# Kernel tuning notes

Measured on AMD Instinct MI355X. Metric: run time of the kernel, lower is better.

Reference implementation:

```python
import jax, jax.numpy as jnp
import numpy as np

N, D, E = 16384, 256, 8
H = D // 2  # gate hidden


def setup_inputs() -> dict:
    key = jax.random.key(0)
    ks = jax.random.split(key, 10)
    s = lambda fan_in: 1.0 / np.sqrt(fan_in)
    return {
        "x":   jax.random.normal(ks[0], (N, D), dtype=jnp.float32),
        # gate: Linear(D, D//2) -> ReLU -> Linear(D//2, E) -> Softmax
        "Wg1": jax.random.uniform(ks[1], (D, H), jnp.float32, -s(D), s(D)),
        "bg1": jax.random.uniform(ks[2], (H,), jnp.float32, -s(D), s(D)),
        "Wg2": jax.random.uniform(ks[3], (H, E), jnp.float32, -s(H), s(H)),
        "bg2": jax.random.uniform(ks[4], (E,), jnp.float32, -s(H), s(H)),
        # experts: per-expert Linear(D,D) -> ReLU -> (Dropout eval=identity) -> Linear(D,D)
        "W1": jax.random.uniform(ks[5], (E, D, D), jnp.float32, -s(D), s(D)),
        "b1": jax.random.uniform(ks[6], (E, D), jnp.float32, -s(D), s(D)),
        "W2": jax.random.uniform(ks[7], (E, D, D), jnp.float32, -s(D), s(D)),
        "b2": jax.random.uniform(ks[8], (E, D), jnp.float32, -s(D), s(D)),
    }


def reference(x, Wg1, bg1, Wg2, bg2, W1, b1, W2, b2):
    # gate: [N, E] softmax over experts
    g = jax.nn.softmax(jax.nn.relu(x @ Wg1 + bg1) @ Wg2 + bg2, axis=-1)
    # all experts applied densely via batched GEMMs (fuses the Python loop)
    h = jax.nn.relu(jnp.einsum("nd,edh->neh", x, W1) + b1)  # [N, E, D]
    y = jnp.einsum("neh,ehd->ned", h, W2) + b2              # [N, E, D]
    # weighted combine: sum_e g[n,e] * y[n,e,:]
    return jnp.einsum("ned,ne->nd", y, g)
```

## Files before the change

### kernel.cpp

```cpp
#include <hip/hip_runtime.h>


typedef unsigned short USH;
typedef float f32x4 __attribute__((ext_vector_type(4)));
typedef __bf16 bf16x8 __attribute__((ext_vector_type(8)));

__device__ __forceinline__ USH f2bf(float f) {
  unsigned int u = __float_as_uint(f);
  u += 0x7fffu + ((u >> 16) & 1u);
  return (USH)(u >> 16);
}


__global__ __launch_bounds__(256) void k_prep(
    const float* __restrict__ Wg1,
    const float* __restrict__ W1,
    const float* __restrict__ W2,
    USH* __restrict__ w1f, USH* __restrict__ w2f, USH* __restrict__ wg1f) {
  __shared__ float T[64][65];
  int b = blockIdx.x, tid = threadIdx.x;

  if (b < 128) {
    int e = b >> 4, tl = b & 15;
    int c0 = (tl >> 2) * 64, h0 = (tl & 3) * 64;
    const float* src = W1 + (size_t)e * 65536;
#pragma unroll
    for (int p = 0; p < 4; ++p) {
      int r = p * 16 + (tid >> 4), d4 = (tid & 15) * 4;
      float4 v = *(const float4*)(src + (size_t)(c0 + r) * 256 + h0 + d4);
      T[r][d4] = v.x; T[r][d4 + 1] = v.y; T[r][d4 + 2] = v.z; T[r][d4 + 3] = v.w;
    }
    __syncthreads();
#pragma unroll
    for (int p = 0; p < 4; ++p) {
      int hr = p * 16 + (tid >> 4), c4 = (tid & 15) * 4;
      USH w[4];
#pragma unroll
      for (int j = 0; j < 4; ++j) w[j] = f2bf(T[c4 + j][hr]);
      int h = h0 + hr;
      int t = h >> 4, lh = h & 15;
      int kt = c0 >> 6, ch = (c4 >> 5) & 1, q = (c4 >> 3) & 3, u0 = c4 & 7;
      size_t idx = ((size_t)((e * 64 + kt * 16 + t) * 2 + ch)) * 512 + (q * 16 + lh) * 8 + u0;
      *(uint2*)(w1f + idx) = *(const uint2*)w;
    }
  } else if (b < 256) {
    int bp = b - 128;
    int e = bp >> 4, tl = bp & 15;
    int h0 = (tl >> 2) * 64, d0 = (tl & 3) * 64;
    const float* src = W2 + (size_t)e * 65536;
#pragma unroll
    for (int p = 0; p < 4; ++p) {
      int r = p * 16 + (tid >> 4), d4 = (tid & 15) * 4;
      float4 v = *(const float4*)(src + (size_t)(h0 + r) * 256 + d0 + d4);
      T[r][d4] = v.x; T[r][d4 + 1] = v.y; T[r][d4 + 2] = v.z; T[r][d4 + 3] = v.w;
    }
    __syncthreads();
#pragma unroll
    for (int p = 0; p < 4; ++p) {
      int dr = p * 16 + (tid >> 4), h4 = (tid & 15) * 4;
      USH w[4];
#pragma unroll
      for (int j = 0; j < 4; ++j) w[j] = f2bf(T[h4 + j][dr]);
      int d = d0 + dr;
      int t = d >> 4, ld = d & 15;
      int ht = h0 >> 6, ch = (h4 >> 5) & 1, q = (h4 >> 3) & 3, u0 = h4 & 7;
      size_t idx = ((size_t)((e * 64 + ht * 16 + t) * 2 + ch)) * 512 + (q * 16 + ld) * 8 + u0;
      *(uint2*)(w2f + idx) = *(const uint2*)w;
    }
  } else {
    int bp = b - 256;
    int c0 = (bp >> 1) * 64, h0 = (bp & 1) * 64;
#pragma unroll
    for (int p = 0; p < 4; ++p) {
      int r = p * 16 + (tid >> 4), d4 = (tid & 15) * 4;
      float4 v = *(const float4*)(Wg1 + (size_t)(c0 + r) * 128 + h0 + d4);
      T[r][d4] = v.x; T[r][d4 + 1] = v.y; T[r][d4 + 2] = v.z; T[r][d4 + 3] = v.w;
    }
    __syncthreads();
#pragma unroll
    for (int p = 0; p < 4; ++p) {
      int hr = p * 16 + (tid >> 4), c4 = (tid & 15) * 4;
      USH w[4];
#pragma unroll
      for (int j = 0; j < 4; ++j) w[j] = f2bf(T[c4 + j][hr]);
      int h = h0 + hr;
      int t = h >> 4, lh = h & 15;
      int kt = c0 >> 6, ch = (c4 >> 5) & 1, q = (c4 >> 3) & 3, u0 = c4 & 7;
      size_t idx = ((size_t)((kt * 8 + t) * 2 + ch)) * 512 + (q * 16 + lh) * 8 + u0;
      *(uint2*)(wg1f + idx) = *(const uint2*)w;
    }
  }
}


__global__ __launch_bounds__(1024)
__attribute__((amdgpu_waves_per_eu(4, 4)))
void k_moe(
    const float* __restrict__ x,
    const USH* __restrict__ w1f,
    const USH* __restrict__ w2f,
    const USH* __restrict__ wg1f,
    const float* __restrict__ wg2,
    const float* __restrict__ bg1,
    const float* __restrict__ bg2,
    const float* __restrict__ b1,
    const float* __restrict__ b2,
    float* __restrict__ out) {
  __shared__ __align__(16) USH xs[4 * 64 * 64];
  __shared__ __align__(16) USH Hs[2][64 * 256];
  __shared__ float b1s[2048];
  __shared__ float b2s[2048];
  __shared__ float gse[512];
  __shared__ float wg2t[8 * 132];
  __shared__ float lgg[512];
  __shared__ float bg1s[128];
  __shared__ float bg2g[8];

  int tid = threadIdx.x;
  int wave = tid >> 6, lane = tid & 63;
  int quad = lane >> 4, l16 = lane & 15;
  int sw = l16 & 7;
  int own = wave >> 1;
  int nh = wave & 1;
  int rowBase = blockIdx.x * 64;
  float* hgs = (float*)&Hs[0][0];

#pragma unroll
  for (int it = 0; it < 2; ++it) {
    int i = it * 1024 + tid;
    int kt = i >> 9, rem = i & 511;
    int r = rem >> 3, slot = rem & 7;
    int c8 = slot ^ (r & 7);
    const float* sp = x + (size_t)(rowBase + r) * 256 + kt * 64 + c8 * 8;
    float4 a = *(const float4*)sp;
    float4 bq = *(const float4*)(sp + 4);
    USH v[8];
    v[0] = f2bf(a.x);  v[1] = f2bf(a.y);  v[2] = f2bf(a.z);  v[3] = f2bf(a.w);
    v[4] = f2bf(bq.x); v[5] = f2bf(bq.y); v[6] = f2bf(bq.z); v[7] = f2bf(bq.w);
    *(uint4*)(xs + (size_t)i * 8) = *(const uint4*)v;
  }
#pragma unroll
  for (int t = 0; t < 2; ++t) {
    b1s[t * 1024 + tid] = b1[t * 1024 + tid];
    b2s[t * 1024 + tid] = b2[t * 1024 + tid];
  }
  wg2t[(tid & 7) * 132 + (tid >> 3)] = wg2[tid & 1023];
  if (tid < 128) bg1s[tid] = bg1[tid];
  if (tid < 8) bg2g[tid] = bg2[tid];

  bf16x8 wra[8], wrb[8];
  auto LDWH = [&](bf16x8* dst, const USH* We, int tb) {
#pragma unroll
    for (int k = 0; k < 2; ++k)
#pragma unroll
      for (int c = 0; c < 2; ++c)
#pragma unroll
        for (int i = 0; i < 2; ++i)
          dst[k * 4 + c * 2 + i] = *(const bf16x8*)(
              We + (size_t)(((tb + k) * 16 + own * 2 + i) * 2 + c) * 512 + lane * 8);
  };
  LDWH(wra, w1f, 0);
  LDWH(wrb, w1f, 2);

  asm volatile("s_waitcnt lgkmcnt(0)" ::: "memory");
  __builtin_amdgcn_s_barrier();

  if (tid < 512) {
    f32x4 hg4[4] = {};
#pragma unroll
    for (int kt = 0; kt < 4; ++kt)
#pragma unroll
      for (int c = 0; c < 2; ++c) {
        int cs = ((c * 4 + quad) ^ sw) * 8;
        bf16x8 av = *(const bf16x8*)(wg1f + (size_t)((kt * 8 + wave) * 2 + c) * 512 + lane * 8);
        bf16x8 bv[4];
#pragma unroll
        for (int j = 0; j < 4; ++j)
          bv[j] = *(const bf16x8*)(xs + kt * 4096 + (j * 16 + l16) * 64 + cs);
#pragma unroll
        for (int j = 0; j < 4; ++j)
          hg4[j] = __builtin_amdgcn_mfma_f32_16x16x32_bf16(av, bv[j], hg4[j], 0, 0, 0);
      }
    int hb = wave * 16 + quad * 4;
    int slotbase = wave * 4 + quad;
#pragma unroll
    for (int j = 0; j < 4; ++j) {
      int n = j * 16 + l16;
      int slot = slotbase ^ (n & 7);
      f32x4 v;
#pragma unroll
      for (int r = 0; r < 4; ++r) v[r] = fmaxf(hg4[j][r] + bg1s[hb + r], 0.0f);
      *(f32x4*)(hgs + n * 128 + slot * 4) = v;
    }
  }
  asm volatile("s_waitcnt lgkmcnt(0)" ::: "memory");
  __builtin_amdgcn_s_barrier();

  if (tid < 512) {
    int n = tid >> 3, eg = tid & 7;
    float s = bg2g[eg];
#pragma unroll
    for (int k4 = 0; k4 < 32; ++k4) {
      int slot = k4 ^ (n & 7);
      f32x4 hv = *(const f32x4*)(hgs + n * 128 + slot * 4);
      const float* wv = wg2t + eg * 132 + k4 * 4;
      s += hv[0] * wv[0]; s += hv[1] * wv[1]; s += hv[2] * wv[2]; s += hv[3] * wv[3];
    }
    lgg[tid] = s;
  }
  asm volatile("s_waitcnt lgkmcnt(0)" ::: "memory");
  __builtin_amdgcn_s_barrier();

  if (tid < 64) {
    float l[8]; float m = -1e30f;
#pragma unroll
    for (int e = 0; e < 8; ++e) { l[e] = lgg[tid * 8 + e]; m = fmaxf(m, l[e]); }
    float s = 0.0f;
#pragma unroll
    for (int e = 0; e < 8; ++e) { l[e] = expf(l[e] - m); s += l[e]; }
    float inv = 1.0f / s;
#pragma unroll
    for (int e = 0; e < 8; ++e) gse[e * 64 + tid] = l[e] * inv;
  }
  asm volatile("s_waitcnt lgkmcnt(0)" ::: "memory");
  __builtin_amdgcn_s_barrier();

  f32x4 oacc[2][2] = {};

#pragma unroll 1
  for (int e = 0; e < 8; ++e) {
    const USH* W2e = w2f + (size_t)e * 65536;
    const USH* W1n = w1f + (size_t)((e + 1) & 7) * 65536;
    f32x4 hacc[2][2] = {};

#pragma unroll
    for (int kt = 0; kt < 2; ++kt)
#pragma unroll
      for (int c = 0; c < 2; ++c) {
        int cs = ((c * 4 + quad) ^ sw) * 8;
        bf16x8 bv[2];
#pragma unroll
        for (int j = 0; j < 2; ++j)
          bv[j] = *(const bf16x8*)(xs + kt * 4096 + (nh * 32 + j * 16 + l16) * 64 + cs);
#pragma unroll
        for (int i = 0; i < 2; ++i)
#pragma unroll
          for (int j = 0; j < 2; ++j)
            hacc[i][j] = __builtin_amdgcn_mfma_f32_16x16x32_bf16(
                wra[kt * 4 + c * 2 + i], bv[j], hacc[i][j], 0, 0, 0);
      }
    LDWH(wra, W2e, 0);
#pragma unroll
    for (int kt = 2; kt < 4; ++kt)
#pragma unroll
      for (int c = 0; c < 2; ++c) {
        int cs = ((c * 4 + quad) ^ sw) * 8;
        bf16x8 bv[2];
#pragma unroll
        for (int j = 0; j < 2; ++j)
          bv[j] = *(const bf16x8*)(xs + kt * 4096 + (nh * 32 + j * 16 + l16) * 64 + cs);
#pragma unroll
        for (int i = 0; i < 2; ++i)
#pragma unroll
          for (int j = 0; j < 2; ++j)
            hacc[i][j] = __builtin_amdgcn_mfma_f32_16x16x32_bf16(
                wrb[(kt - 2) * 4 + c * 2 + i], bv[j], hacc[i][j], 0, 0, 0);
      }
    LDWH(wrb, W2e, 2);

    USH* Hb = &Hs[e & 1][0];
#pragma unroll
    for (int i = 0; i < 2; ++i) {
      int hb = own * 32 + i * 16 + quad * 4;
      int slot = (hb >> 3) & 7;
      int h64 = hb >> 6;
#pragma unroll
      for (int j = 0; j < 2; ++j) {
        int n = nh * 32 + j * 16 + l16;
        float gg = gse[e * 64 + n];
        USH w4[4];
#pragma unroll
        for (int r = 0; r < 4; ++r)
          w4[r] = f2bf(fmaxf(hacc[i][j][r] + b1s[e * 256 + hb + r], 0.0f) * gg);
        int off = n * 256 + h64 * 64 + ((slot ^ (n & 7)) * 8) + (quad & 1) * 4;
        *(uint2*)(Hb + off) = *(const uint2*)w4;
      }
    }

    asm volatile("s_waitcnt lgkmcnt(0)" ::: "memory");
    __builtin_amdgcn_s_barrier();

#pragma unroll
    for (int ht = 0; ht < 2; ++ht)
#pragma unroll
      for (int c = 0; c < 2; ++c) {
        int cs = ((c * 4 + quad) ^ sw) * 8;
        bf16x8 av[2];
#pragma unroll
        for (int i = 0; i < 2; ++i)
          av[i] = *(const bf16x8*)(Hb + (nh * 32 + i * 16 + l16) * 256 + ht * 64 + cs);
#pragma unroll
        for (int i = 0; i < 2; ++i)
#pragma unroll
          for (int j = 0; j < 2; ++j)
            oacc[i][j] = __builtin_amdgcn_mfma_f32_16x16x32_bf16(
                av[i], wra[ht * 4 + c * 2 + j], oacc[i][j], 0, 0, 0);
      }
    LDWH(wra, W1n, 0);
#pragma unroll
    for (int ht = 2; ht < 4; ++ht)
#pragma unroll
      for (int c = 0; c < 2; ++c) {
        int cs = ((c * 4 + quad) ^ sw) * 8;
        bf16x8 av[2];
#pragma unroll
        for (int i = 0; i < 2; ++i)
          av[i] = *(const bf16x8*)(Hb + (nh * 32 + i * 16 + l16) * 256 + ht * 64 + cs);
#pragma unroll
        for (int i = 0; i < 2; ++i)
#pragma unroll
          for (int j = 0; j < 2; ++j)
            oacc[i][j] = __builtin_amdgcn_mfma_f32_16x16x32_bf16(
                av[i], wrb[(ht - 2) * 4 + c * 2 + j], oacc[i][j], 0, 0, 0);
      }
    LDWH(wrb, W1n, 2);
  }

#pragma unroll
  for (int i = 0; i < 2; ++i)
#pragma unroll
    for (int r = 0; r < 4; ++r) {
      int n = nh * 32 + i * 16 + quad * 4 + r;
      size_t grow = (size_t)(rowBase + n) * 256;
#pragma unroll
      for (int j = 0; j < 2; ++j) {
        int d = own * 32 + j * 16 + l16;
        float bias = 0.0f;
#pragma unroll
        for (int ee = 0; ee < 8; ++ee) bias += gse[ee * 64 + n] * b2s[ee * 256 + d];
        out[grow + d] = oacc[i][j][r] + bias;
      }
    }
}


extern "C" void kernel_launch(void* const* d_in, const int* in_sizes, int n_in,
                              void* d_out, int out_size, void* d_ws, size_t ws_size,
                              hipStream_t stream) {
  const float* x   = (const float*)d_in[0];
  const float* Wg1 = (const float*)d_in[1];
  const float* bg1 = (const float*)d_in[2];
  const float* Wg2 = (const float*)d_in[3];
  const float* bg2 = (const float*)d_in[4];
  const float* W1  = (const float*)d_in[5];
  const float* b1  = (const float*)d_in[6];
  const float* W2  = (const float*)d_in[7];
  const float* b2  = (const float*)d_in[8];
  float* out = (float*)d_out;

  char* ws = (char*)d_ws;
  USH* w1f  = (USH*)(ws + 8388608);
  USH* wg1f = (USH*)(ws + 9437184);
  USH* w2f  = (USH*)(ws + 9502720);

  hipLaunchKernelGGL(k_prep, dim3(264), dim3(256), 0, stream,
                     Wg1, W1, W2, w1f, w2f, wg1f);
  hipLaunchKernelGGL(k_moe, dim3(256), dim3(1024), 0, stream,
                     x, w1f, w2f, wg1f, Wg2, bg1, bg2, b1, b2, out);
}
```

Baseline: 148.9 us.

## Split MoE blocks to 32 rows with 512 threads, doubling grid size

Halves the rows per block from 64 to 32 and the threads per block from 1024 to 512, so the grid grows from 256 to 512 blocks and two blocks can share a CU. Each wave now owns a distinct 32-column slice of the hidden/output dimension rather than pairing waves on row halves. The aim is to fill all CUs on the device and let two blocks overlap their barriers and phases. The cost is that every block loads the full expert weights into registers for only 32 rows, doubling total weight traffic from L2.

Measured after the change: 141.6 us. 1.05x faster.

```diff
diff --git a/kernel.cpp b/kernel.cpp
--- a/kernel.cpp
+++ b/kernel.cpp
@@ -93,9 +93,7 @@
 }
 
 
-__global__ __launch_bounds__(1024)
-__attribute__((amdgpu_waves_per_eu(4, 4)))
-void k_moe(
+__global__ __launch_bounds__(512, 2) void k_moe(
     const float* __restrict__ x,
     const USH* __restrict__ w1f,
     const USH* __restrict__ w2f,
@@ -106,13 +104,13 @@
     const float* __restrict__ b1,
     const float* __restrict__ b2,
     float* __restrict__ out) {
-  __shared__ __align__(16) USH xs[4 * 64 * 64];
-  __shared__ __align__(16) USH Hs[2][64 * 256];
+  __shared__ __align__(16) USH xs[4 * 32 * 64];
+  __shared__ __align__(16) USH Hs[2][32 * 256];
   __shared__ float b1s[2048];
   __shared__ float b2s[2048];
-  __shared__ float gse[512];
+  __shared__ float gse[256];
   __shared__ float wg2t[8 * 132];
-  __shared__ float lgg[512];
+  __shared__ float lgg[256];
   __shared__ float bg1s[128];
   __shared__ float bg2g[8];
 
@@ -120,15 +118,13 @@
   int wave = tid >> 6, lane = tid & 63;
   int quad = lane >> 4, l16 = lane & 15;
   int sw = l16 & 7;
-  int own = wave >> 1;
-  int nh = wave & 1;
-  int rowBase = blockIdx.x * 64;
+  int rowBase = blockIdx.x * 32;
   float* hgs = (float*)&Hs[0][0];
 
 #pragma unroll
   for (int it = 0; it < 2; ++it) {
-    int i = it * 1024 + tid;
-    int kt = i >> 9, rem = i & 511;
+    int i = it * 512 + tid;
+    int kt = i >> 8, rem = i & 255;
     int r = rem >> 3, slot = rem & 7;
     int c8 = slot ^ (r & 7);
     const float* sp = x + (size_t)(rowBase + r) * 256 + kt * 64 + c8 * 8;
@@ -140,11 +136,11 @@
     *(uint4*)(xs + (size_t)i * 8) = *(const uint4*)v;
   }
 #pragma unroll
-  for (int t = 0; t < 2; ++t) {
-    b1s[t * 1024 + tid] = b1[t * 1024 + tid];
-    b2s[t * 1024 + tid] = b2[t * 1024 + tid];
-  }
-  wg2t[(tid & 7) * 132 + (tid >> 3)] = wg2[tid & 1023];
+  for (int t = 0; t < 4; ++t) {
+    b1s[t * 512 + tid] = b1[t * 512 + tid];
+    b2s[t * 512 + tid] = b2[t * 512 + tid];
+  }
+  for (int t = tid; t < 1024; t += 512) wg2t[(t & 7) * 132 + (t >> 3)] = wg2[t];
   if (tid < 128) bg1s[tid] = bg1[tid];
   if (tid < 8) bg2g[tid] = bg2[tid];
 
@@ -157,7 +153,7 @@
 #pragma unroll
         for (int i = 0; i < 2; ++i)
           dst[k * 4 + c * 2 + i] = *(const bf16x8*)(
-              We + (size_t)(((tb + k) * 16 + own * 2 + i) * 2 + c) * 512 + lane * 8);
+              We + (size_t)(((tb + k) * 16 + wave * 2 + i) * 2 + c) * 512 + lane * 8);
   };
   LDWH(wra, w1f, 0);
   LDWH(wrb, w1f, 2);
@@ -165,26 +161,26 @@
   asm volatile("s_waitcnt lgkmcnt(0)" ::: "memory");
   __builtin_amdgcn_s_barrier();
 
-  if (tid < 512) {
-    f32x4 hg4[4] = {};
+  {
+    f32x4 hg4[2] = {};
 #pragma unroll
     for (int kt = 0; kt < 4; ++kt)
 #pragma unroll
       for (int c = 0; c < 2; ++c) {
         int cs = ((c * 4 + quad) ^ sw) * 8;
         bf16x8 av = *(const bf16x8*)(wg1f + (size_t)((kt * 8 + wave) * 2 + c) * 512 + lane * 8);
-        bf16x8 bv[4];
-#pragma unroll
-        for (int j = 0; j < 4; ++j)
-          bv[j] = *(const bf16x8*)(xs + kt * 4096 + (j * 16 + l16) * 64 + cs);
-#pragma unroll
-        for (int j = 0; j < 4; ++j)
+        bf16x8 bv[2];
+#pragma unroll
+        for (int j = 0; j < 2; ++j)
+          bv[j] = *(const bf16x8*)(xs + kt * 2048 + (j * 16 + l16) * 64 + cs);
+#pragma unroll
+        for (int j = 0; j < 2; ++j)
           hg4[j] = __builtin_amdgcn_mfma_f32_16x16x32_bf16(av, bv[j], hg4[j], 0, 0, 0);
       }
     int hb = wave * 16 + quad * 4;
     int slotbase = wave * 4 + quad;
 #pragma unroll
-    for (int j = 0; j < 4; ++j) {
+    for (int j = 0; j < 2; ++j) {
       int n = j * 16 + l16;
       int slot = slotbase ^ (n & 7);
       f32x4 v;
@@ -196,7 +192,7 @@
   asm volatile("s_waitcnt lgkmcnt(0)" ::: "memory");
   __builtin_amdgcn_s_barrier();
 
-  if (tid < 512) {
+  if (tid < 256) {
     int n = tid >> 3, eg = tid & 7;
     float s = bg2g[eg];
 #pragma unroll
@@ -211,7 +207,7 @@
   asm volatile("s_waitcnt lgkmcnt(0)" ::: "memory");
   __builtin_amdgcn_s_barrier();
 
-  if (tid < 64) {
+  if (tid < 32) {
     float l[8]; float m = -1e30f;
 #pragma unroll
     for (int e = 0; e < 8; ++e) { l[e] = lgg[tid * 8 + e]; m = fmaxf(m, l[e]); }
@@ -220,7 +216,7 @@
     for (int e = 0; e < 8; ++e) { l[e] = expf(l[e] - m); s += l[e]; }
     float inv = 1.0f / s;
 #pragma unroll
-    for (int e = 0; e < 8; ++e) gse[e * 64 + tid] = l[e] * inv;
+    for (int e = 0; e < 8; ++e) gse[e * 32 + tid] = l[e] * inv;
   }
   asm volatile("s_waitcnt lgkmcnt(0)" ::: "memory");
   __builtin_amdgcn_s_barrier();
@@ -241,7 +237,7 @@
         bf16x8 bv[2];
 #pragma unroll
         for (int j = 0; j < 2; ++j)
-          bv[j] = *(const bf16x8*)(xs + kt * 4096 + (nh * 32 + j * 16 + l16) * 64 + cs);
+          bv[j] = *(const bf16x8*)(xs + kt * 2048 + (j * 16 + l16) * 64 + cs);
 #pragma unroll
         for (int i = 0; i < 2; ++i)
 #pragma unroll
@@ -258,7 +254,7 @@
         bf16x8 bv[2];
 #pragma unroll
         for (int j = 0; j < 2; ++j)
-          bv[j] = *(const bf16x8*)(xs + kt * 4096 + (nh * 32 + j * 16 + l16) * 64 + cs);
+          bv[j] = *(const bf16x8*)(xs + kt * 2048 + (j * 16 + l16) * 64 + cs);
 #pragma unroll
         for (int i = 0; i < 2; ++i)
 #pragma unroll
@@ -271,18 +267,17 @@
     USH* Hb = &Hs[e & 1][0];
 #pragma unroll
     for (int i = 0; i < 2; ++i) {
-      int hb = own * 32 + i * 16 + quad * 4;
-      int slot = (hb >> 3) & 7;
-      int h64 = hb >> 6;
+      int slot = (wave & 1) * 4 + i * 2 + (quad >> 1);
+      int hb = wave * 32 + i * 16 + quad * 4;
 #pragma unroll
       for (int j = 0; j < 2; ++j) {
-        int n = nh * 32 + j * 16 + l16;
-        float gg = gse[e * 64 + n];
+        int n = j * 16 + l16;
+        float gg = gse[e * 32 + n];
         USH w4[4];
 #pragma unroll
         for (int r = 0; r < 4; ++r)
           w4[r] = f2bf(fmaxf(hacc[i][j][r] + b1s[e * 256 + hb + r], 0.0f) * gg);
-        int off = n * 256 + h64 * 64 + ((slot ^ (n & 7)) * 8) + (quad & 1) * 4;
+        int off = n * 256 + (wave >> 1) * 64 + ((slot ^ (n & 7)) * 8) + (quad & 1) * 4;
         *(uint2*)(Hb + off) = *(const uint2*)w4;
       }
     }
@@ -298,7 +293,7 @@
         bf16x8 av[2];
 #pragma unroll
         for (int i = 0; i < 2; ++i)
-          av[i] = *(const bf16x8*)(Hb + (nh * 32 + i * 16 + l16) * 256 + ht * 64 + cs);
+          av[i] = *(const bf16x8*)(Hb + (i * 16 + l16) * 256 + ht * 64 + cs);
 #pragma unroll
         for (int i = 0; i < 2; ++i)
 #pragma unroll
@@ -315,7 +310,7 @@
         bf16x8 av[2];
 #pragma unroll
         for (int i = 0; i < 2; ++i)
-          av[i] = *(const bf16x8*)(Hb + (nh * 32 + i * 16 + l16) * 256 + ht * 64 + cs);
+          av[i] = *(const bf16x8*)(Hb + (i * 16 + l16) * 256 + ht * 64 + cs);
 #pragma unroll
         for (int i = 0; i < 2; ++i)
 #pragma unroll
@@ -330,14 +325,14 @@
   for (int i = 0; i < 2; ++i)
 #pragma unroll
     for (int r = 0; r < 4; ++r) {
-      int n = nh * 32 + i * 16 + quad * 4 + r;
+      int n = i * 16 + quad * 4 + r;
       size_t grow = (size_t)(rowBase + n) * 256;
 #pragma unroll
       for (int j = 0; j < 2; ++j) {
-        int d = own * 32 + j * 16 + l16;
+        int d = wave * 32 + j * 16 + l16;
         float bias = 0.0f;
 #pragma unroll
-        for (int ee = 0; ee < 8; ++ee) bias += gse[ee * 64 + n] * b2s[ee * 256 + d];
+        for (int ee = 0; ee < 8; ++ee) bias += gse[ee * 32 + n] * b2s[ee * 256 + d];
         out[grow + d] = oacc[i][j][r] + bias;
       }
     }
@@ -365,6 +360,6 @@
 
   hipLaunchKernelGGL(k_prep, dim3(264), dim3(256), 0, stream,
                      Wg1, W1, W2, w1f, w2f, wg1f);
-  hipLaunchKernelGGL(k_moe, dim3(256), dim3(1024), 0, stream,
+  hipLaunchKernelGGL(k_moe, dim3(512), dim3(512), 0, stream,
                      x, w1f, w2f, wg1f, Wg2, bg1, bg2, b1, b2, out);
 }
```
